# Kernel optimization log

Hardware: AMD Instinct MI355X
Metric: run time of the kernel (lower is better)

Reference implementation:

```python
import jax, jax.numpy as jnp
import numpy as np

N = 200000
D = 256  # node_dim

def setup_inputs() -> dict:
    key = jax.random.key(0)
    k0, k1, kw, kb = jax.random.split(key, 4)
    var_v0 = jax.random.normal(k0, (N, D), dtype=jnp.float32)
    var_v1 = jax.random.normal(k1, (N, D), dtype=jnp.float32)
    W = jax.random.normal(kw, (2 * D, 2 * D), dtype=jnp.float32) * 0.02
    b = jax.random.normal(kb, (2 * D,), dtype=jnp.float32) * 0.02
    return {"var_v0": var_v0, "var_v1": var_v1, "W": W, "b": b}

def reference(var_v0, var_v1, W, b):
    # cat along feature dim -> [N, 2D]
    catted = jnp.concatenate([var_v0, var_v1], axis=1)
    # Linear (torch convention: x @ W.T + b) then ReLU
    activated = jax.nn.relu(catted @ W.T + b)
    # sum-pool over all nodes -> [1, 2D] (replaces the python loop of adds)
    readout = jnp.sum(activated, axis=0, keepdims=True)
    return readout
```

## Files before the change

### kernel.cpp

```cpp
#include <hip/hip_runtime.h>
#include <hip/hip_bf16.h>


typedef __bf16 bf16x8 __attribute__((ext_vector_type(8)));
typedef float  f32x4  __attribute__((ext_vector_type(4)));

#define BM   128
#define BN   128
#define BK   32
#define NK   16
#define LDA  56
#define SLOTS 128
#define NCB  4

static __device__ __forceinline__ unsigned short f2bf(float f) {
    __bf16 h = (__bf16)f;
    return __builtin_bit_cast(unsigned short, h);
}

__global__ __launch_bounds__(256, 2) void fused_gemm_pool(
    const float* __restrict__ v0, const float* __restrict__ v1,
    const float* __restrict__ W,  const float* __restrict__ b,
    float* __restrict__ partial, int N, int numRB)
{
    __shared__ unsigned short As[2][BM * LDA];
    __shared__ unsigned short Bs[2][BN * LDA];
    __shared__ float ldsPart[4][64];

    int bid   = blockIdx.x;
    int group = bid >> 5;
    int xcd   = bid & 7;
    int cb    = (bid >> 3) & 3;
    int slot  = group * 8 + xcd;

    int tid  = threadIdx.x;
    int wid  = tid >> 6;
    int lane = tid & 63;
    int wr   = wid >> 1;
    int wc   = wid & 1;
    int l15  = lane & 15;
    int l4   = lane >> 4;

    float bv[4];
    #pragma unroll
    for (int nf = 0; nf < 4; ++nf) bv[nf] = b[cb * 128 + wc * 64 + nf * 16 + l15];

    float csum[4] = {0.f, 0.f, 0.f, 0.f};

    float4 ra[4], rbv[4];

    for (int rbk = slot; rbk < numRB; rbk += SLOTS) {
        int rowBase = rbk * BM;

        f32x4 acc[4][4];
        #pragma unroll
        for (int mf = 0; mf < 4; ++mf)
            #pragma unroll
            for (int nf = 0; nf < 4; ++nf)
                acc[mf][nf] = (f32x4){0.f, 0.f, 0.f, 0.f};

        auto loadRegs = [&](int kt) {
            int k0 = kt * BK;
            const float* srcA = (k0 < 256) ? (v0 + (size_t)rowBase * 256 + k0)
                                           : (v1 + (size_t)rowBase * 256 + (k0 - 256));
            #pragma unroll
            for (int i = 0; i < 4; ++i) {
                int idx = tid + i * 256;
                int row = idx >> 3, kq = idx & 7;
                float4 f = {0.f, 0.f, 0.f, 0.f};
                if (rowBase + row < N)
                    f = *(const float4*)(srcA + (size_t)row * 256 + kq * 4);
                ra[i] = f;
                rbv[i] = *(const float4*)(W + (size_t)(cb * 128 + row) * 512 + k0 + kq * 4);
            }
        };
        auto writeLds = [&](int buf) {
            #pragma unroll
            for (int i = 0; i < 4; ++i) {
                int idx = tid + i * 256;
                int row = idx >> 3, kq = idx & 7;
                union { unsigned short u[4]; uint2 v; } pa, pb;
                pa.u[0] = f2bf(ra[i].x);  pa.u[1] = f2bf(ra[i].y);
                pa.u[2] = f2bf(ra[i].z);  pa.u[3] = f2bf(ra[i].w);
                pb.u[0] = f2bf(rbv[i].x); pb.u[1] = f2bf(rbv[i].y);
                pb.u[2] = f2bf(rbv[i].z); pb.u[3] = f2bf(rbv[i].w);
                *(uint2*)&As[buf][row * LDA + kq * 4] = pa.v;
                *(uint2*)&Bs[buf][row * LDA + kq * 4] = pb.v;
            }
        };
        auto compute = [&](int buf) {
            bf16x8 af[4], bfr[4];
            #pragma unroll
            for (int mf = 0; mf < 4; ++mf) {
                int r = wr * 64 + mf * 16 + l15;
                af[mf] = *(const bf16x8*)&As[buf][r * LDA + l4 * 8];
            }
            #pragma unroll
            for (int nf = 0; nf < 4; ++nf) {
                int c = wc * 64 + nf * 16 + l15;
                bfr[nf] = *(const bf16x8*)&Bs[buf][c * LDA + l4 * 8];
            }
            #pragma unroll
            for (int mf = 0; mf < 4; ++mf)
                #pragma unroll
                for (int nf = 0; nf < 4; ++nf)
                    acc[mf][nf] = __builtin_amdgcn_mfma_f32_16x16x32_bf16(
                        af[mf], bfr[nf], acc[mf][nf], 0, 0, 0);
        };

        loadRegs(0);
        __syncthreads();
        writeLds(0);
        int cur = 0;
        for (int kt = 0; kt < NK; ++kt) {
            if (kt + 1 < NK) loadRegs(kt + 1);
            __syncthreads();
            compute(cur);
            if (kt + 1 < NK) writeLds(cur ^ 1);
            cur ^= 1;
        }

        #pragma unroll
        for (int nf = 0; nf < 4; ++nf) {
            float bb = bv[nf];
            #pragma unroll
            for (int mf = 0; mf < 4; ++mf) {
                int rbase = rowBase + wr * 64 + mf * 16 + l4 * 4;
                #pragma unroll
                for (int r = 0; r < 4; ++r) {
                    float v = acc[mf][nf][r] + bb;
                    v = fmaxf(v, 0.f);
                    if (rbase + r < N) csum[nf] += v;
                }
            }
        }
    }

    #pragma unroll
    for (int nf = 0; nf < 4; ++nf) {
        float s = csum[nf];
        s += __shfl_xor(s, 16);
        s += __shfl_xor(s, 32);
        if (lane < 16) ldsPart[wid][nf * 16 + lane] = s;
    }
    __syncthreads();
    if (tid < 128) {
        int half = tid >> 6, c = tid & 63;
        float v = ldsPart[half][c] + ldsPart[half + 2][c];
        partial[(size_t)slot * 512 + cb * 128 + tid] = v;
    }
}

__global__ void reduce_partials(const float* __restrict__ partial, float* __restrict__ out)
{
    int c = blockIdx.x * blockDim.x + threadIdx.x;
    if (c < 512) {
        float s = 0.f;
        for (int s2 = 0; s2 < SLOTS; ++s2) s += partial[(size_t)s2 * 512 + c];
        out[c] = s;
    }
}

extern "C" void kernel_launch(void* const* d_in, const int* in_sizes, int n_in,
                              void* d_out, int out_size, void* d_ws, size_t ws_size,
                              hipStream_t stream)
{
    const float* v0 = (const float*)d_in[0];
    const float* v1 = (const float*)d_in[1];
    const float* W  = (const float*)d_in[2];
    const float* b  = (const float*)d_in[3];
    float* out      = (float*)d_out;
    float* partial  = (float*)d_ws;

    int N = in_sizes[0] / 256;
    int numRB = (N + BM - 1) / BM;

    fused_gemm_pool<<<dim3(SLOTS * NCB), dim3(256), 0, stream>>>(
        v0, v1, W, b, partial, N, numRB);
    reduce_partials<<<dim3(2), dim3(256), 0, stream>>>(partial, out);
}
```

Before: 221.8 us.

## Pre-convert W to bf16, stage it via global_load_lds, swizzle LDS, deepen A prefetch

Result: slower. 247.3 us (+11.5%).

```diff
diff --git a/kernel.cpp b/kernel.cpp
--- a/kernel.cpp
+++ b/kernel.cpp
@@ -4,27 +4,47 @@
 
 typedef __bf16 bf16x8 __attribute__((ext_vector_type(8)));
 typedef float  f32x4  __attribute__((ext_vector_type(4)));
-
-#define BM   128
-#define BN   128
-#define BK   32
-#define NK   16
-#define LDA  56
+typedef unsigned short u16x4 __attribute__((ext_vector_type(4)));
+
+#define BM 128
+#define BN 128
+#define BK 32
+#define NK 16
 #define SLOTS 128
-#define NCB  4
-
+#define NCB 4
+
+static __device__ __forceinline__ int swz(int r) { return (r & 3) ^ ((r >> 2) & 3); }
 static __device__ __forceinline__ unsigned short f2bf(float f) {
-    __bf16 h = (__bf16)f;
-    return __builtin_bit_cast(unsigned short, h);
-}
-
-__global__ __launch_bounds__(256, 2) void fused_gemm_pool(
+    return __builtin_bit_cast(unsigned short, (__bf16)f);
+}
+static __device__ __forceinline__ bf16x8 pack8(float4 a, float4 b) {
+    bf16x8 o;
+    o[0] = (__bf16)a.x; o[1] = (__bf16)a.y; o[2] = (__bf16)a.z; o[3] = (__bf16)a.w;
+    o[4] = (__bf16)b.x; o[5] = (__bf16)b.y; o[6] = (__bf16)b.z; o[7] = (__bf16)b.w;
+    return o;
+}
+
+#define GLDS16(G, L) __builtin_amdgcn_global_load_lds(                       \
+    (const __attribute__((address_space(1))) void*)(G),                     \
+    (__attribute__((address_space(3))) void*)(L), 16, 0, 0)
+
+__global__ void conv_w_bf16(const float* __restrict__ W, unsigned short* __restrict__ Wb) {
+    int idx = (blockIdx.x * blockDim.x + threadIdx.x) * 4;
+    float4 f = *(const float4*)(W + idx);
+    u16x4 p;
+    p[0] = f2bf(f.x); p[1] = f2bf(f.y); p[2] = f2bf(f.z); p[3] = f2bf(f.w);
+    *(u16x4*)(Wb + idx) = p;
+}
+
+template<bool WBF16>
+__global__ __launch_bounds__(256) void fused_gemm_pool(
     const float* __restrict__ v0, const float* __restrict__ v1,
-    const float* __restrict__ W,  const float* __restrict__ b,
+    const float* __restrict__ Wf, const unsigned short* __restrict__ Wb,
+    const float* __restrict__ b,
     float* __restrict__ partial, int N, int numRB)
 {
-    __shared__ unsigned short As[2][BM * LDA];
-    __shared__ unsigned short Bs[2][BN * LDA];
+    __shared__ unsigned short As[2][BM * BK];
+    __shared__ unsigned short Bs[2][BN * BK];
     __shared__ float ldsPart[4][64];
 
     int bid   = blockIdx.x;
@@ -33,21 +53,39 @@
     int cb    = (bid >> 3) & 3;
     int slot  = group * 8 + xcd;
 
-    int tid  = threadIdx.x;
-    int wid  = tid >> 6;
-    int lane = tid & 63;
-    int wr   = wid >> 1;
-    int wc   = wid & 1;
-    int l15  = lane & 15;
-    int l4   = lane >> 4;
+    int tid = threadIdx.x, wid = tid >> 6, lane = tid & 63;
+    int wr = wid >> 1, wc = wid & 1, l15 = lane & 15, l4 = lane >> 4;
+
+    int rowA[2], offAg[2], offAw[2], offBg[2], offBw[2], offBgl[2];
+    #pragma unroll
+    for (int i = 0; i < 2; ++i) {
+        int m = tid + i * 256;
+        int r = m >> 2, c = m & 3;
+        rowA[i]  = r;
+        offAg[i] = r * 256 + c * 8;
+        offAw[i] = r * BK + ((c ^ swz(r)) * 8);
+        offBg[i] = (cb * 128 + r) * 512 + c * 8;
+        offBw[i] = offAw[i];
+        int mu = (wid + i * 4) * 64 + lane;
+        int br = mu >> 2, bc = mu & 3;
+        offBgl[i] = (cb * 128 + br) * 512 + ((bc ^ swz(br)) * 8);
+    }
+    int offAf[4], offBf[4];
+    #pragma unroll
+    for (int f = 0; f < 4; ++f) {
+        int r = wr * 64 + f * 16 + l15;
+        offAf[f] = r * BK + ((l4 ^ swz(r)) * 8);
+        int cc = wc * 64 + f * 16 + l15;
+        offBf[f] = cc * BK + ((l4 ^ swz(cc)) * 8);
+    }
 
     float bv[4];
     #pragma unroll
     for (int nf = 0; nf < 4; ++nf) bv[nf] = b[cb * 128 + wc * 64 + nf * 16 + l15];
 
     float csum[4] = {0.f, 0.f, 0.f, 0.f};
-
-    float4 ra[4], rbv[4];
+    float4 rA[2][4];
+    float4 rB[2][4];
 
     for (int rbk = slot; rbk < numRB; rbk += SLOTS) {
         int rowBase = rbk * BM;
@@ -59,65 +97,80 @@
             for (int nf = 0; nf < 4; ++nf)
                 acc[mf][nf] = (f32x4){0.f, 0.f, 0.f, 0.f};
 
-        auto loadRegs = [&](int kt) {
-            int k0 = kt * BK;
-            const float* srcA = (k0 < 256) ? (v0 + (size_t)rowBase * 256 + k0)
-                                           : (v1 + (size_t)rowBase * 256 + (k0 - 256));
-            #pragma unroll
-            for (int i = 0; i < 4; ++i) {
-                int idx = tid + i * 256;
-                int row = idx >> 3, kq = idx & 7;
-                float4 f = {0.f, 0.f, 0.f, 0.f};
-                if (rowBase + row < N)
-                    f = *(const float4*)(srcA + (size_t)row * 256 + kq * 4);
-                ra[i] = f;
-                rbv[i] = *(const float4*)(W + (size_t)(cb * 128 + row) * 512 + k0 + kq * 4);
-            }
-        };
-        auto writeLds = [&](int buf) {
-            #pragma unroll
-            for (int i = 0; i < 4; ++i) {
-                int idx = tid + i * 256;
-                int row = idx >> 3, kq = idx & 7;
-                union { unsigned short u[4]; uint2 v; } pa, pb;
-                pa.u[0] = f2bf(ra[i].x);  pa.u[1] = f2bf(ra[i].y);
-                pa.u[2] = f2bf(ra[i].z);  pa.u[3] = f2bf(ra[i].w);
-                pb.u[0] = f2bf(rbv[i].x); pb.u[1] = f2bf(rbv[i].y);
-                pb.u[2] = f2bf(rbv[i].z); pb.u[3] = f2bf(rbv[i].w);
-                *(uint2*)&As[buf][row * LDA + kq * 4] = pa.v;
-                *(uint2*)&Bs[buf][row * LDA + kq * 4] = pb.v;
-            }
-        };
-        auto compute = [&](int buf) {
-            bf16x8 af[4], bfr[4];
-            #pragma unroll
-            for (int mf = 0; mf < 4; ++mf) {
-                int r = wr * 64 + mf * 16 + l15;
-                af[mf] = *(const bf16x8*)&As[buf][r * LDA + l4 * 8];
-            }
-            #pragma unroll
-            for (int nf = 0; nf < 4; ++nf) {
-                int c = wc * 64 + nf * 16 + l15;
-                bfr[nf] = *(const bf16x8*)&Bs[buf][c * LDA + l4 * 8];
-            }
+        auto loadA = [&](int kt, int s) {
+            const float* src = (kt < 8) ? v0 : v1;
+            int k0 = (kt & 7) * 32;
+            #pragma unroll
+            for (int i = 0; i < 2; ++i) {
+                float4 f0 = {0,0,0,0}, f1 = {0,0,0,0};
+                if (rowBase + rowA[i] < N) {
+                    const float* p = src + (size_t)rowBase * 256 + offAg[i] + k0;
+                    f0 = *(const float4*)p;
+                    f1 = *(const float4*)(p + 4);
+                }
+                rA[s][i * 2]     = f0;
+                rA[s][i * 2 + 1] = f1;
+            }
+        };
+        auto writeA = [&](int s, int buf) {
+            #pragma unroll
+            for (int i = 0; i < 2; ++i)
+                *(bf16x8*)&As[buf][offAw[i]] = pack8(rA[s][i * 2], rA[s][i * 2 + 1]);
+        };
+        auto stageBglds = [&](int kt, int buf) {
+            int k0 = kt * 32;
+            #pragma unroll
+            for (int j = 0; j < 2; ++j)
+                GLDS16(Wb + offBgl[j] + k0, &Bs[buf][(wid + j * 4) * 512]);
+        };
+        auto loadB = [&](int kt, int s) {
+            int k0 = kt * 32;
+            #pragma unroll
+            for (int i = 0; i < 2; ++i) {
+                const float* p = Wf + offBg[i] + k0;
+                rB[s][i * 2]     = *(const float4*)p;
+                rB[s][i * 2 + 1] = *(const float4*)(p + 4);
+            }
+        };
+        auto writeB = [&](int s, int buf) {
+            #pragma unroll
+            for (int i = 0; i < 2; ++i)
+                *(bf16x8*)&Bs[buf][offBw[i]] = pack8(rB[s][i * 2], rB[s][i * 2 + 1]);
+        };
+
+        if constexpr (WBF16) stageBglds(0, 0); else loadB(0, 0);
+        loadA(0, 0);
+        loadA(1, 1);
+        if constexpr (!WBF16) loadB(1, 1);
+        writeA(0, 0);
+        if constexpr (!WBF16) writeB(0, 0);
+
+        #pragma unroll
+        for (int kt = 0; kt < NK; ++kt) {
+            int cur = kt & 1;
+            __syncthreads();
+            if constexpr (WBF16) {
+                if (kt + 1 < NK) stageBglds(kt + 1, cur ^ 1);
+            }
+            if (kt + 2 < NK) {
+                loadA(kt + 2, cur);
+                if constexpr (!WBF16) loadB(kt + 2, cur);
+            }
+            bf16x8 af[4], bf[4];
+            #pragma unroll
+            for (int f = 0; f < 4; ++f) af[f] = *(const bf16x8*)&As[cur][offAf[f]];
+            #pragma unroll
+            for (int f = 0; f < 4; ++f) bf[f] = *(const bf16x8*)&Bs[cur][offBf[f]];
             #pragma unroll
             for (int mf = 0; mf < 4; ++mf)
                 #pragma unroll
                 for (int nf = 0; nf < 4; ++nf)
                     acc[mf][nf] = __builtin_amdgcn_mfma_f32_16x16x32_bf16(
-                        af[mf], bfr[nf], acc[mf][nf], 0, 0, 0);
-        };
-
-        loadRegs(0);
-        __syncthreads();
-        writeLds(0);
-        int cur = 0;
-        for (int kt = 0; kt < NK; ++kt) {
-            if (kt + 1 < NK) loadRegs(kt + 1);
-            __syncthreads();
-            compute(cur);
-            if (kt + 1 < NK) writeLds(cur ^ 1);
-            cur ^= 1;
+                        af[mf], bf[nf], acc[mf][nf], 0, 0, 0);
+            if (kt + 1 < NK) {
+                writeA(cur ^ 1, cur ^ 1);
+                if constexpr (!WBF16) writeB(cur ^ 1, cur ^ 1);
+            }
         }
 
         #pragma unroll
@@ -128,8 +181,7 @@
                 int rbase = rowBase + wr * 64 + mf * 16 + l4 * 4;
                 #pragma unroll
                 for (int r = 0; r < 4; ++r) {
-                    float v = acc[mf][nf][r] + bb;
-                    v = fmaxf(v, 0.f);
+                    float v = fmaxf(acc[mf][nf][r] + bb, 0.f);
                     if (rbase + r < N) csum[nf] += v;
                 }
             }
@@ -167,15 +219,27 @@
 {
     const float* v0 = (const float*)d_in[0];
     const float* v1 = (const float*)d_in[1];
-    const float* W  = (const float*)d_in[2];
+    const float* Wf = (const float*)d_in[2];
     const float* b  = (const float*)d_in[3];
     float* out      = (float*)d_out;
-    float* partial  = (float*)d_ws;
 
     int N = in_sizes[0] / 256;
     int numRB = (N + BM - 1) / BM;
 
-    fused_gemm_pool<<<dim3(SLOTS * NCB), dim3(256), 0, stream>>>(
-        v0, v1, W, b, partial, N, numRB);
-    reduce_partials<<<dim3(2), dim3(256), 0, stream>>>(partial, out);
-}
+    size_t wbytes = (size_t)512 * 512 * sizeof(unsigned short);
+    size_t pbytes = (size_t)SLOTS * 512 * sizeof(float);
+
+    if (ws_size >= wbytes + pbytes) {
+        unsigned short* Wb = (unsigned short*)d_ws;
+        float* partial = (float*)((char*)d_ws + wbytes);
+        conv_w_bf16<<<dim3(256), dim3(256), 0, stream>>>(Wf, Wb);
+        fused_gemm_pool<true><<<dim3(SLOTS * NCB), dim3(256), 0, stream>>>(
+            v0, v1, Wf, Wb, b, partial, N, numRB);
+        reduce_partials<<<dim3(2), dim3(256), 0, stream>>>(partial, out);
+    } else {
+        float* partial = (float*)d_ws;
+        fused_gemm_pool<false><<<dim3(SLOTS * NCB), dim3(256), 0, stream>>>(
+            v0, v1, Wf, nullptr, b, partial, N, numRB);
+        reduce_partials<<<dim3(2), dim3(256), 0, stream>>>(partial, out);
+    }
+}
```

## Keep W slice resident in swizzled LDS and stream A directly from global

Applied to the files above, without the earlier changes.

Result: slower. 828.5 us (+273.5%).

```diff
diff --git a/kernel.cpp b/kernel.cpp
--- a/kernel.cpp
+++ b/kernel.cpp
@@ -5,131 +5,105 @@
 typedef __bf16 bf16x8 __attribute__((ext_vector_type(8)));
 typedef float  f32x4  __attribute__((ext_vector_type(4)));
 
-#define BM   128
-#define BN   128
-#define BK   32
-#define NK   16
-#define LDA  56
+#define BM 256
+#define BN 64
+#define NK 16
 #define SLOTS 128
-#define NCB  4
+#define NCB 8
 
-static __device__ __forceinline__ unsigned short f2bf(float f) {
-    __bf16 h = (__bf16)f;
-    return __builtin_bit_cast(unsigned short, h);
+static __device__ __forceinline__ bf16x8 pack8(float4 a, float4 b) {
+    bf16x8 o;
+    o[0] = (__bf16)a.x; o[1] = (__bf16)a.y; o[2] = (__bf16)a.z; o[3] = (__bf16)a.w;
+    o[4] = (__bf16)b.x; o[5] = (__bf16)b.y; o[6] = (__bf16)b.z; o[7] = (__bf16)b.w;
+    return o;
 }
 
-__global__ __launch_bounds__(256, 2) void fused_gemm_pool(
+__global__ __launch_bounds__(512, 4) void fused_gemm_pool(
     const float* __restrict__ v0, const float* __restrict__ v1,
     const float* __restrict__ W,  const float* __restrict__ b,
     float* __restrict__ partial, int N, int numRB)
 {
-    __shared__ unsigned short As[2][BM * LDA];
-    __shared__ unsigned short Bs[2][BN * LDA];
-    __shared__ float ldsPart[4][64];
+    __shared__ unsigned short Ws[BN * 512];
+    __shared__ float ldsPart[8][64];
 
-    int bid   = blockIdx.x;
-    int group = bid >> 5;
-    int xcd   = bid & 7;
-    int cb    = (bid >> 3) & 3;
-    int slot  = group * 8 + xcd;
+    int bid  = blockIdx.x;
+    int xcd  = bid & 7;
+    int cb   = (bid >> 3) & 7;
+    int grp  = bid >> 6;
+    int slot = grp * 8 + xcd;
 
-    int tid  = threadIdx.x;
-    int wid  = tid >> 6;
-    int lane = tid & 63;
-    int wr   = wid >> 1;
-    int wc   = wid & 1;
-    int l15  = lane & 15;
-    int l4   = lane >> 4;
+    int tid = threadIdx.x, wid = tid >> 6, lane = tid & 63;
+    int l15 = lane & 15, l4 = lane >> 4;
+
+    #pragma unroll
+    for (int i = 0; i < 8; ++i) {
+        int m = tid + i * 512;
+        int row = m >> 6, chunk = m & 63;
+        const float* wsrc = W + (size_t)(cb * 64 + row) * 512 + chunk * 8;
+        float4 f0 = *(const float4*)wsrc;
+        float4 f1 = *(const float4*)(wsrc + 4);
+        *(bf16x8*)&Ws[row * 512 + ((chunk ^ (row & 7)) * 8)] = pack8(f0, f1);
+    }
+    __syncthreads();
+
+    int s3 = l15 & 7;
+    int bBase[4];
+    #pragma unroll
+    for (int nf = 0; nf < 4; ++nf) bBase[nf] = (nf * 16 + l15) * 512;
 
     float bv[4];
     #pragma unroll
-    for (int nf = 0; nf < 4; ++nf) bv[nf] = b[cb * 128 + wc * 64 + nf * 16 + l15];
+    for (int nf = 0; nf < 4; ++nf) bv[nf] = b[cb * 64 + nf * 16 + l15];
 
     float csum[4] = {0.f, 0.f, 0.f, 0.f};
 
-    float4 ra[4], rbv[4];
+    for (int rbk = slot; rbk < numRB; rbk += SLOTS) {
+        int rb0 = rbk * BM + wid * 32;
+        int r0 = rb0 + l15, r1 = rb0 + 16 + l15;
+        bool ok0 = r0 < N, ok1 = r1 < N;
+        const float* pa00 = v0 + (size_t)r0 * 256 + l4 * 8;
+        const float* pa01 = v1 + (size_t)r0 * 256 + l4 * 8;
+        const float* pa10 = v0 + (size_t)r1 * 256 + l4 * 8;
+        const float* pa11 = v1 + (size_t)r1 * 256 + l4 * 8;
 
-    for (int rbk = slot; rbk < numRB; rbk += SLOTS) {
-        int rowBase = rbk * BM;
-
-        f32x4 acc[4][4];
+        f32x4 acc[2][4];
         #pragma unroll
-        for (int mf = 0; mf < 4; ++mf)
+        for (int mf = 0; mf < 2; ++mf)
             #pragma unroll
             for (int nf = 0; nf < 4; ++nf)
                 acc[mf][nf] = (f32x4){0.f, 0.f, 0.f, 0.f};
 
-        auto loadRegs = [&](int kt) {
-            int k0 = kt * BK;
-            const float* srcA = (k0 < 256) ? (v0 + (size_t)rowBase * 256 + k0)
-                                           : (v1 + (size_t)rowBase * 256 + (k0 - 256));
+        #pragma unroll
+        for (int kt = 0; kt < NK; ++kt) {
+            const int k0 = (kt & 7) * 32;
+            float4 f00 = {0,0,0,0}, f01 = {0,0,0,0};
+            float4 f10 = {0,0,0,0}, f11 = {0,0,0,0};
+            const float* p0 = (kt < 8) ? pa00 : pa01;
+            const float* p1 = (kt < 8) ? pa10 : pa11;
+            if (ok0) { f00 = *(const float4*)(p0 + k0); f01 = *(const float4*)(p0 + k0 + 4); }
+            if (ok1) { f10 = *(const float4*)(p1 + k0); f11 = *(const float4*)(p1 + k0 + 4); }
+            bf16x8 a0 = pack8(f00, f01);
+            bf16x8 a1 = pack8(f10, f11);
+            bf16x8 bfr[4];
             #pragma unroll
-            for (int i = 0; i < 4; ++i) {
-                int idx = tid + i * 256;
-                int row = idx >> 3, kq = idx & 7;
-                float4 f = {0.f, 0.f, 0.f, 0.f};
-                if (rowBase + row < N)
-                    f = *(const float4*)(srcA + (size_t)row * 256 + kq * 4);
-                ra[i] = f;
-                rbv[i] = *(const float4*)(W + (size_t)(cb * 128 + row) * 512 + k0 + kq * 4);
-            }
-        };
-        auto writeLds = [&](int buf) {
-            #pragma unroll
-            for (int i = 0; i < 4; ++i) {
-                int idx = tid + i * 256;
-                int row = idx >> 3, kq = idx & 7;
-                union { unsigned short u[4]; uint2 v; } pa, pb;
-                pa.u[0] = f2bf(ra[i].x);  pa.u[1] = f2bf(ra[i].y);
-                pa.u[2] = f2bf(ra[i].z);  pa.u[3] = f2bf(ra[i].w);
-                pb.u[0] = f2bf(rbv[i].x); pb.u[1] = f2bf(rbv[i].y);
-                pb.u[2] = f2bf(rbv[i].z); pb.u[3] = f2bf(rbv[i].w);
-                *(uint2*)&As[buf][row * LDA + kq * 4] = pa.v;
-                *(uint2*)&Bs[buf][row * LDA + kq * 4] = pb.v;
-            }
-        };
-        auto compute = [&](int buf) {
-            bf16x8 af[4], bfr[4];
-            #pragma unroll
-            for (int mf = 0; mf < 4; ++mf) {
-                int r = wr * 64 + mf * 16 + l15;
-                af[mf] = *(const bf16x8*)&As[buf][r * LDA + l4 * 8];
-            }
+            for (int nf = 0; nf < 4; ++nf)
+                bfr[nf] = *(const bf16x8*)&Ws[bBase[nf] + (((kt * 4 + l4) ^ s3) * 8)];
             #pragma unroll
             for (int nf = 0; nf < 4; ++nf) {
-                int c = wc * 64 + nf * 16 + l15;
-                bfr[nf] = *(const bf16x8*)&Bs[buf][c * LDA + l4 * 8];
+                acc[0][nf] = __builtin_amdgcn_mfma_f32_16x16x32_bf16(a0, bfr[nf], acc[0][nf], 0, 0, 0);
+                acc[1][nf] = __builtin_amdgcn_mfma_f32_16x16x32_bf16(a1, bfr[nf], acc[1][nf], 0, 0, 0);
             }
-            #pragma unroll
-            for (int mf = 0; mf < 4; ++mf)
-                #pragma unroll
-                for (int nf = 0; nf < 4; ++nf)
-                    acc[mf][nf] = __builtin_amdgcn_mfma_f32_16x16x32_bf16(
-                        af[mf], bfr[nf], acc[mf][nf], 0, 0, 0);
-        };
-
-        loadRegs(0);
-        __syncthreads();
-        writeLds(0);
-        int cur = 0;
-        for (int kt = 0; kt < NK; ++kt) {
-            if (kt + 1 < NK) loadRegs(kt + 1);
-            __syncthreads();
-            compute(cur);
-            if (kt + 1 < NK) writeLds(cur ^ 1);
-            cur ^= 1;
         }
 
         #pragma unroll
         for (int nf = 0; nf < 4; ++nf) {
             float bb = bv[nf];
             #pragma unroll
-            for (int mf = 0; mf < 4; ++mf) {
-                int rbase = rowBase + wr * 64 + mf * 16 + l4 * 4;
+            for (int mf = 0; mf < 2; ++mf) {
+                int rbase = rb0 + mf * 16 + l4 * 4;
                 #pragma unroll
                 for (int r = 0; r < 4; ++r) {
-                    float v = acc[mf][nf][r] + bb;
-                    v = fmaxf(v, 0.f);
+                    float v = fmaxf(acc[mf][nf][r] + bb, 0.f);
                     if (rbase + r < N) csum[nf] += v;
                 }
             }
@@ -144,10 +118,11 @@
         if (lane < 16) ldsPart[wid][nf * 16 + lane] = s;
     }
     __syncthreads();
-    if (tid < 128) {
-        int half = tid >> 6, c = tid & 63;
-        float v = ldsPart[half][c] + ldsPart[half + 2][c];
-        partial[(size_t)slot * 512 + cb * 128 + tid] = v;
+    if (tid < 64) {
+        float s = 0.f;
+        #pragma unroll
+        for (int w = 0; w < 8; ++w) s += ldsPart[w][tid];
+        partial[(size_t)slot * 512 + cb * 64 + tid] = s;
     }
 }
 
@@ -156,7 +131,7 @@
     int c = blockIdx.x * blockDim.x + threadIdx.x;
     if (c < 512) {
         float s = 0.f;
-        for (int s2 = 0; s2 < SLOTS; ++s2) s += partial[(size_t)s2 * 512 + c];
+        for (int i = 0; i < SLOTS; ++i) s += partial[(size_t)i * 512 + c];
         out[c] = s;
     }
 }
@@ -175,7 +150,7 @@
     int N = in_sizes[0] / 256;
     int numRB = (N + BM - 1) / BM;
 
-    fused_gemm_pool<<<dim3(SLOTS * NCB), dim3(256), 0, stream>>>(
+    fused_gemm_pool<<<dim3(SLOTS * NCB), dim3(512), 0, stream>>>(
         v0, v1, W, b, partial, N, numRB);
     reduce_partials<<<dim3(2), dim3(256), 0, stream>>>(partial, out);
 }
```
